# Kernel tuning notes

Hardware: AMD Instinct MI355X
Metric: run time of the kernel (lower is better)

The kernel has to match this reference:

```python
import jax, jax.numpy as jnp
import numpy as np

D_MODEL = 2048
NUM_HEADS = 16
D_K = D_MODEL // NUM_HEADS


def setup_inputs() -> dict:
    key = jax.random.key(0)
    ks = jax.random.split(key, 12)
    B, S, D = 2, 2048, D_MODEL
    s = 1.0 / np.sqrt(D)
    return {
        "q": jax.random.normal(ks[0], (B, S, D), jnp.float32),
        "k": jax.random.normal(ks[1], (B, S, D), jnp.float32),
        "v": jax.random.normal(ks[2], (B, S, D), jnp.float32),
        "Wq": jax.random.normal(ks[3], (D, D), jnp.float32) * s,
        "bq": jax.random.normal(ks[4], (D,), jnp.float32) * 0.01,
        "Wk": jax.random.normal(ks[5], (D, D), jnp.float32) * s,
        "bk": jax.random.normal(ks[6], (D,), jnp.float32) * 0.01,
        "Wv": jax.random.normal(ks[7], (D, D), jnp.float32) * s,
        "bv": jax.random.normal(ks[8], (D,), jnp.float32) * 0.01,
        "Wo": jax.random.normal(ks[9], (D, D), jnp.float32) * s,
        "bo": jax.random.normal(ks[10], (D,), jnp.float32) * 0.01,
    }


def reference(q, k, v, Wq, bq, Wk, bk, Wv, bv, Wo, bo):
    B, S, D = q.shape
    H, dk = NUM_HEADS, D_K

    def proj(x, W, b):
        # Linear then split heads -> [B, H, S, dk]
        y = jnp.einsum('bsd,df->bsf', x, W) + b
        return y.reshape(B, -1, H, dk).transpose(0, 2, 1, 3)

    Q = proj(q, Wq, bq)
    K = proj(k, Wk, bk)
    V = proj(v, Wv, bv)

    scores = jnp.einsum('bhqd,bhkd->bhqk', Q, K) / jnp.sqrt(jnp.float32(dk))
    attn = jax.nn.softmax(scores, axis=-1)  # dropout is identity (eval)
    out = jnp.einsum('bhqk,bhkd->bhqd', attn, V)
    out = out.transpose(0, 2, 1, 3).reshape(B, -1, D)
    return jnp.einsum('bsd,df->bsf', out, Wo) + bo
```

## Files before the change

### kernel.cpp

```cpp
#include <hip/hip_runtime.h>
#include <hip/hip_bf16.h>
#include <stdint.h>

typedef float  f32x4  __attribute__((ext_vector_type(4)));
typedef float  f32x16 __attribute__((ext_vector_type(16)));
typedef short  s16x8  __attribute__((ext_vector_type(8)));

#define D_MODEL 2048
#define NHEADS  16
#define DK      128
#define BATCH   2
#define SEQ     2048
#define MROWS   (BATCH*SEQ)

__device__ __forceinline__ unsigned short f2bf(float f) {
  union { float f; unsigned int u; } v; v.f = f;
  unsigned int r = v.u + 0x7FFFu + ((v.u >> 16) & 1u);
  return (unsigned short)(r >> 16);
}

__device__ __forceinline__ unsigned int packbf_c(float lo, float hi) {
  __hip_bfloat16 l = __float2bfloat16(lo);
  __hip_bfloat16 h = __float2bfloat16(hi);
  unsigned short lu, hu;
  __builtin_memcpy(&lu, &l, 2);
  __builtin_memcpy(&hu, &h, 2);
  return (unsigned int)lu | ((unsigned int)hu << 16);
}

__device__ __forceinline__ void async16(const void* g, void* l) {
  __builtin_amdgcn_global_load_lds(
      (const __attribute__((address_space(1))) unsigned int*)g,
      (__attribute__((address_space(3))) unsigned int*)l,
      16, 0, 0);
}

__global__ __launch_bounds__(256) void f2b3_kernel(const float* __restrict__ q,
                                                   const float* __restrict__ k,
                                                   const float* __restrict__ v,
                                                   unsigned short* __restrict__ qb,
                                                   unsigned short* __restrict__ kb,
                                                   unsigned short* __restrict__ vb) {
  const float* s; unsigned short* d;
  switch (blockIdx.y) {
    case 0:  s = q; d = qb; break;
    case 1:  s = k; d = kb; break;
    default: s = v; d = vb; break;
  }
  int i = blockIdx.x * 256 + threadIdx.x;
  const float4* s4 = (const float4*)s;
  float4 a = s4[2*i];
  float4 b = s4[2*i+1];
  s16x8 o;
  o[0] = (short)f2bf(a.x); o[1] = (short)f2bf(a.y);
  o[2] = (short)f2bf(a.z); o[3] = (short)f2bf(a.w);
  o[4] = (short)f2bf(b.x); o[5] = (short)f2bf(b.y);
  o[6] = (short)f2bf(b.z); o[7] = (short)f2bf(b.w);
  *(s16x8*)(d + 8*(size_t)i) = o;
}

__global__ __launch_bounds__(256) void wtrans_kernel(const float* __restrict__ Wq,
                                                     const float* __restrict__ Wk,
                                                     const float* __restrict__ Wv,
                                                     const float* __restrict__ Wo,
                                                     unsigned short* __restrict__ WqT,
                                                     unsigned short* __restrict__ WkT,
                                                     unsigned short* __restrict__ WvT,
                                                     unsigned short* __restrict__ WoT) {
  const float* W; unsigned short* Wt;
  switch (blockIdx.z) {
    case 0:  W = Wq; Wt = WqT; break;
    case 1:  W = Wk; Wt = WkT; break;
    case 2:  W = Wv; Wt = WvT; break;
    default: W = Wo; Wt = WoT; break;
  }
  __shared__ float tl[32][33];
  int x = threadIdx.x, y = threadIdx.y;
  int n0 = blockIdx.x * 32, k0 = blockIdx.y * 32;
  #pragma unroll
  for (int j = 0; j < 32; j += 8)
    tl[y + j][x] = W[(size_t)(k0 + y + j) * D_MODEL + n0 + x];
  __syncthreads();
  #pragma unroll
  for (int j = 0; j < 32; j += 8)
    Wt[(size_t)(n0 + y + j) * D_MODEL + k0 + x] = f2bf(tl[x][y + j]);
}

__device__ __forceinline__ void gemm3b_core(const unsigned short* __restrict__ A,
                                            const unsigned short* __restrict__ Bt,
                                            const float* __restrict__ bias,
                                            void* __restrict__ Cout,
                                            int N, int K, int mode, float scale,
                                            int m0, int n0, char* lds) {
  const int t  = threadIdx.x;
  const int l  = t & 63, w = t >> 6;
  const int wm = w >> 1, wn = w & 1;
  const int lr = l & 15, lg = l >> 4;

  auto STAGE = [&](int slot, int kt) {
    char* Ad = lds + slot*49152;
    char* Bd = lds + slot*49152 + 32768;
    #pragma unroll
    for (int i = 0; i < 4; ++i) {
      int c = t + 512*i;
      int row = c >> 3, crs = (c & 7) ^ (row & 7);
      async16(A + (size_t)(m0 + row)*K + kt*64 + crs*8, Ad + c*16);
    }
    #pragma unroll
    for (int i = 0; i < 2; ++i) {
      int c = t + 512*i;
      int row = c >> 3, crs = (c & 7) ^ (row & 7);
      async16(Bt + (size_t)(n0 + row)*K + kt*64 + crs*8, Bd + c*16);
    }
  };

  const int NT = K >> 6;
  STAGE(0, 0);
  STAGE(1, 1);
  asm volatile("s_waitcnt vmcnt(6)" ::: "memory");
  __builtin_amdgcn_s_barrier();

  f32x4 acc[4][4] = {};

  for (int kt = 0; kt < NT; ++kt) {
    if (kt + 2 < NT) STAGE((kt + 2) % 3, kt + 2);
    const char* Ac = lds + (kt % 3)*49152;
    const char* Bc = lds + (kt % 3)*49152 + 32768;

    #pragma unroll
    for (int ks = 0; ks < 2; ++ks) {
      const int cb = ks*64 + lg*16;
      s16x8 af[4], bf[4];
      #pragma unroll
      for (int mf = 0; mf < 4; ++mf) {
        int row = wm*64 + mf*16 + lr;
        af[mf] = *(const s16x8*)(Ac + row*128 + (cb ^ ((row & 7) << 4)));
      }
      #pragma unroll
      for (int nf = 0; nf < 4; ++nf) {
        int row = wn*64 + nf*16 + lr;
        bf[nf] = *(const s16x8*)(Bc + row*128 + (cb ^ ((row & 7) << 4)));
      }
      __builtin_amdgcn_s_setprio(1);
      #pragma unroll
      for (int mf = 0; mf < 4; ++mf)
        #pragma unroll
        for (int nf = 0; nf < 4; ++nf)
          acc[mf][nf] = __builtin_amdgcn_mfma_f32_16x16x32_bf16(af[mf], bf[nf], acc[mf][nf], 0, 0, 0);
      __builtin_amdgcn_s_setprio(0);
    }

    if (kt + 1 < NT) {
      if (kt + 2 < NT) asm volatile("s_waitcnt vmcnt(6)" ::: "memory");
      else             asm volatile("s_waitcnt vmcnt(0)" ::: "memory");
      __builtin_amdgcn_s_barrier();
    }
  }

  if (mode == 0) {
    float* C = (float*)Cout;
    #pragma unroll
    for (int nf = 0; nf < 4; ++nf) {
      int col = n0 + wn*64 + nf*16 + lr;
      float bv = bias[col];
      #pragma unroll
      for (int mf = 0; mf < 4; ++mf) {
        int rowb = m0 + wm*64 + mf*16 + lg*4;
        #pragma unroll
        for (int r = 0; r < 4; ++r)
          C[(size_t)(rowb + r)*N + col] = (acc[mf][nf][r] + bv) * scale;
      }
    }
  } else if (mode == 1) {
    unsigned short* C = (unsigned short*)Cout;
    #pragma unroll
    for (int nf = 0; nf < 4; ++nf) {
      int col = n0 + wn*64 + nf*16 + lr;
      float bv = bias[col];
      int h = col >> 7, dkk = col & 127;
      #pragma unroll
      for (int mf = 0; mf < 4; ++mf) {
        int rowb = m0 + wm*64 + mf*16 + lg*4;
        #pragma unroll
        for (int r = 0; r < 4; ++r) {
          int row = rowb + r;
          int b = row >> 11, s = row & 2047;
          C[((size_t)((b*NHEADS + h)*SEQ + s))*DK + dkk] = f2bf((acc[mf][nf][r] + bv) * scale);
        }
      }
    }
  } else {
    unsigned short* C = (unsigned short*)Cout;
    #pragma unroll
    for (int nf = 0; nf < 4; ++nf) {
      int col = n0 + wn*64 + nf*16 + lr;
      float bv = bias[col];
      int h = col >> 7, dkk = col & 127;
      #pragma unroll
      for (int mf = 0; mf < 4; ++mf) {
        int rowb = m0 + wm*64 + mf*16 + lg*4;
        #pragma unroll
        for (int r = 0; r < 4; ++r) {
          int row = rowb + r;
          int b = row >> 11, s = row & 2047;
          C[((size_t)((b*NHEADS + h)*DK + dkk))*SEQ + s] = f2bf((acc[mf][nf][r] + bv) * scale);
        }
      }
    }
  }
}

__device__ __forceinline__ void swz_mn(int& m0, int& n0) {
  int lin = blockIdx.y * 16 + blockIdx.x;
  int xcd = lin & 7;
  int pos = lin >> 3;
  n0 = (xcd*2 + (pos & 1)) * 128;
  m0 = (pos >> 1) * 256;
}

__global__ __launch_bounds__(512) void gemm256_qkv(const unsigned short* __restrict__ qb,
                                                   const unsigned short* __restrict__ kb,
                                                   const unsigned short* __restrict__ vb,
                                                   const unsigned short* __restrict__ WT,
                                                   const float* __restrict__ bq,
                                                   const float* __restrict__ bk,
                                                   const float* __restrict__ bv,
                                                   unsigned short* __restrict__ Hout,
                                                   float qscale) {
  __shared__ char lds[147456];
  const int z = blockIdx.z;
  const unsigned short* A = (z == 0) ? qb : (z == 1) ? kb : vb;
  const float* bias       = (z == 0) ? bq : (z == 1) ? bk : bv;
  const float scale       = (z == 0) ? qscale : 1.0f;
  const int   mode        = (z == 2) ? 2 : 1;
  const unsigned short* Bt = WT + (size_t)z * D_MODEL * D_MODEL;
  unsigned short* Cout     = Hout + (size_t)z * MROWS * D_MODEL;
  int m0, n0; swz_mn(m0, n0);
  gemm3b_core(A, Bt, bias, Cout, D_MODEL, D_MODEL, mode, scale, m0, n0, lds);
}

__global__ __launch_bounds__(512) void gemm256_out(const unsigned short* __restrict__ A,
                                                   const unsigned short* __restrict__ Bt,
                                                   const float* __restrict__ bias,
                                                   float* __restrict__ Cout) {
  __shared__ char lds[147456];
  int m0, n0; swz_mn(m0, n0);
  gemm3b_core(A, Bt, bias, Cout, D_MODEL, D_MODEL, 0, 1.0f, m0, n0, lds);
}

__global__ __launch_bounds__(256, 2) void attn_kernel(const unsigned short* __restrict__ Q,
                                                      const unsigned short* __restrict__ K,
                                                      const unsigned short* __restrict__ Vt_g,
                                                      unsigned short* __restrict__ O) {
  __shared__ char lds[64*256 + 2*16384];
  unsigned short* Kl = (unsigned short*)lds;

  const int t  = threadIdx.x;
  const int l  = t & 63, w = t >> 6;
  const int q_ = l & 31, hi = l >> 5;
  const int bh = blockIdx.y;
  const int b  = bh >> 4, h = bh & 15;
  const int q0 = blockIdx.x * 128;

  const unsigned short* Qp = Q    + (size_t)bh * SEQ * DK;
  const unsigned short* Kp = K    + (size_t)bh * SEQ * DK;
  const unsigned short* Vp = Vt_g + (size_t)bh * DK * SEQ;

  const int qrow = q0 + w*32 + q_;
  s16x8 aq[8];
  #pragma unroll
  for (int kk = 0; kk < 8; ++kk)
    aq[kk] = *(const s16x8*)(Qp + (size_t)qrow*DK + kk*16 + hi*8);

  f32x16 accO[4] = {};
  float m = -INFINITY, L = 0.f;

  const int NT = SEQ/64;

  auto stageK = [&](int kv0) {
    #pragma unroll
    for (int i = 0; i < 4; ++i) {
      int c   = t + 256*i;
      int row = c >> 4;
      int sb  = ((c & 15) << 4) ^ ((row & 15) << 4);
      async16((const char*)(Kp + (size_t)(kv0 + row)*DK) + sb, (char*)Kl + c*16);
    }
  };
  auto stageV = [&](int kv0, int buf) {
    char* Vd = lds + 16384 + buf*16384;
    #pragma unroll
    for (int i = 0; i < 4; ++i) {
      int c   = t + 256*i;
      int row = c >> 3;
      int sb  = ((c & 7) << 4) ^ ((row & 7) << 4);
      async16((const char*)(Vp + (size_t)row*SEQ + kv0) + sb, Vd + c*16);
    }
  };

  stageK(0);
  stageV(0, 0);
  asm volatile("" ::: "memory");

  for (int tt = 0; tt < NT; ++tt) {
    __syncthreads();

    f32x16 S0 = {}, S1 = {};
    __builtin_amdgcn_s_setprio(1);
    #pragma unroll
    for (int t2 = 0; t2 < 2; ++t2) {
      int krow = t2*32 + q_;
      const char* kb = (const char*)Kl + krow*256;
      int swz = (krow & 15) << 4;
      #pragma unroll
      for (int kk = 0; kk < 8; ++kk) {
        s16x8 kf = *(const s16x8*)(kb + ((kk*32 + hi*16) ^ swz));
        if (t2 == 0) S0 = __builtin_amdgcn_mfma_f32_32x32x16_bf16(kf, aq[kk], S0, 0, 0, 0);
        else         S1 = __builtin_amdgcn_mfma_f32_32x32x16_bf16(kf, aq[kk], S1, 0, 0, 0);
      }
    }
    __builtin_amdgcn_s_setprio(0);
    __syncthreads();

    if (tt + 1 < NT) {
      stageK((tt + 1) * 64);
      stageV((tt + 1) * 64, (tt + 1) & 1);
      asm volatile("" ::: "memory");
    }

    f32x16 mx;
    #pragma unroll
    for (int r = 0; r < 16; ++r) mx[r] = fmaxf(S0[r], S1[r]);
    float m8_[8];
    #pragma unroll
    for (int r = 0; r < 8; ++r) m8_[r] = fmaxf(mx[r], mx[r+8]);
    float m4a = fmaxf(m8_[0], m8_[4]), m4b = fmaxf(m8_[1], m8_[5]);
    float m4c = fmaxf(m8_[2], m8_[6]), m4d = fmaxf(m8_[3], m8_[7]);
    float pmax = fmaxf(fmaxf(m4a, m4b), fmaxf(m4c, m4d));
    pmax = fmaxf(pmax, __shfl_xor(pmax, 32, 64));

    if (!__all(pmax <= m + 11.0f)) {
      float mnew = fmaxf(m, pmax);
      float corr = exp2f(m - mnew);
      m = mnew;
      L *= corr;
      #pragma unroll
      for (int sub = 0; sub < 4; ++sub)
        #pragma unroll
        for (int r = 0; r < 16; ++r) accO[sub][r] *= corr;
    }

    float rs0 = 0.f, rs1 = 0.f, rs2 = 0.f, rs3 = 0.f;
    #pragma unroll
    for (int r = 0; r < 4; ++r) {
      float a0 = exp2f(S0[r]    - m); S0[r]    = a0; rs0 += a0;
      float a1 = exp2f(S0[r+4]  - m); S0[r+4]  = a1; rs1 += a1;
      float a2 = exp2f(S0[r+8]  - m); S0[r+8]  = a2; rs2 += a2;
      float a3 = exp2f(S0[r+12] - m); S0[r+12] = a3; rs3 += a3;
      float b0 = exp2f(S1[r]    - m); S1[r]    = b0; rs0 += b0;
      float b1 = exp2f(S1[r+4]  - m); S1[r+4]  = b1; rs1 += b1;
      float b2 = exp2f(S1[r+8]  - m); S1[r+8]  = b2; rs2 += b2;
      float b3 = exp2f(S1[r+12] - m); S1[r+12] = b3; rs3 += b3;
    }
    float rs = (rs0 + rs1) + (rs2 + rs3);
    rs += __shfl_xor(rs, 32, 64);
    L += rs;

    s16x8 PB[4];
    #pragma unroll
    for (int t2 = 0; t2 < 2; ++t2) {
      #pragma unroll
      for (int half = 0; half < 2; ++half) {
        int bse = half*8;
        unsigned int pkA01, pkA23, pkB01, pkB23;
        if (t2 == 0) {
          pkA01 = packbf_c(S0[bse+0], S0[bse+1]);
          pkA23 = packbf_c(S0[bse+2], S0[bse+3]);
          pkB01 = packbf_c(S0[bse+4], S0[bse+5]);
          pkB23 = packbf_c(S0[bse+6], S0[bse+7]);
        } else {
          pkA01 = packbf_c(S1[bse+0], S1[bse+1]);
          pkA23 = packbf_c(S1[bse+2], S1[bse+3]);
          pkB01 = packbf_c(S1[bse+4], S1[bse+5]);
          pkB23 = packbf_c(S1[bse+6], S1[bse+7]);
        }
        unsigned int xA01 = __shfl_xor(pkA01, 32, 64);
        unsigned int xA23 = __shfl_xor(pkA23, 32, 64);
        unsigned int xB01 = __shfl_xor(pkB01, 32, 64);
        unsigned int xB23 = __shfl_xor(pkB23, 32, 64);
        union { unsigned int u[4]; s16x8 v; } f;
        f.u[0] = hi ? xB01 : pkA01;
        f.u[1] = hi ? xB23 : pkA23;
        f.u[2] = hi ? pkB01 : xA01;
        f.u[3] = hi ? pkB23 : xA23;
        PB[t2*2 + half] = f.v;
      }
    }

    const char* Vc = lds + 16384 + (tt & 1)*16384;
    __builtin_amdgcn_s_setprio(1);
    #pragma unroll
    for (int sub = 0; sub < 4; ++sub) {
      int row = sub*32 + q_;
      const char* vb2 = Vc + row*128;
      int swz = (row & 7) << 4;
      #pragma unroll
      for (int kk = 0; kk < 4; ++kk) {
        s16x8 vf = *(const s16x8*)(vb2 + ((kk*32 + hi*16) ^ swz));
        accO[sub] = __builtin_amdgcn_mfma_f32_32x32x16_bf16(vf, PB[kk], accO[sub], 0, 0, 0);
      }
    }
    __builtin_amdgcn_s_setprio(0);
  }

  __syncthreads();
  unsigned short* Ob = (unsigned short*)lds + (size_t)w*4096;
  float inv = 1.0f / L;
  #pragma unroll
  for (int sub = 0; sub < 4; ++sub)
    #pragma unroll
    for (int j = 0; j < 8; ++j) {
      unsigned int pw = packbf_c(accO[sub][2*j]*inv, accO[sub][2*j+1]*inv);
      int dv = sub*32 + (j&1)*2 + ((j>>1)*8) + 4*hi;
      *(unsigned int*)((char*)Ob + q_*256 + ((dv*2) ^ ((q_ & 15) << 4))) = pw;
    }
  asm volatile("s_waitcnt lgkmcnt(0)" ::: "memory");
  size_t gbase = ((size_t)(b*SEQ + q0 + w*32 + q_))*D_MODEL + h*DK;
  #pragma unroll
  for (int p = 0; p < 8; ++p) {
    int chunk = hi + 2*p;
    s16x8 ov = *(const s16x8*)((char*)Ob + q_*256 + ((chunk*16) ^ ((q_ & 15) << 4)));
    *(s16x8*)(O + gbase + chunk*8) = ov;
  }
}

extern "C" void kernel_launch(void* const* d_in, const int* in_sizes, int n_in,
                              void* d_out, int out_size, void* d_ws, size_t ws_size,
                              hipStream_t stream) {
  const float* q  = (const float*)d_in[0];
  const float* k  = (const float*)d_in[1];
  const float* v  = (const float*)d_in[2];
  const float* Wq = (const float*)d_in[3];
  const float* bq = (const float*)d_in[4];
  const float* Wk = (const float*)d_in[5];
  const float* bk = (const float*)d_in[6];
  const float* Wv = (const float*)d_in[7];
  const float* bv = (const float*)d_in[8];
  const float* Wo = (const float*)d_in[9];
  const float* bo = (const float*)d_in[10];
  float* out = (float*)d_out;

  char* ws = (char*)d_ws;
  const size_t SZT = (size_t)MROWS * D_MODEL * 2;
  const size_t SZW = (size_t)D_MODEL * D_MODEL * 2;

  unsigned short* qb  = (unsigned short*)(ws);
  unsigned short* kb  = (unsigned short*)(ws + SZT);
  unsigned short* vb  = (unsigned short*)(ws + 2*SZT);
  unsigned short* WqT = (unsigned short*)(ws + 3*SZT);
  unsigned short* WkT = (unsigned short*)(ws + 3*SZT + SZW);
  unsigned short* WvT = (unsigned short*)(ws + 3*SZT + 2*SZW);
  unsigned short* WoT = (unsigned short*)(ws + 3*SZT + 3*SZW);
  unsigned short* Qh  = (unsigned short*)(ws + 3*SZT + 4*SZW);
  unsigned short* Kh  = (unsigned short*)(ws + 4*SZT + 4*SZW);
  unsigned short* Vh  = (unsigned short*)(ws + 5*SZT + 4*SZW);
  unsigned short* Oc  = qb;

  const int n8 = MROWS * D_MODEL / 8;
  f2b3_kernel<<<dim3(n8/256, 3), 256, 0, stream>>>(q, k, v, qb, kb, vb);
  wtrans_kernel<<<dim3(64, 64, 4), dim3(32, 8), 0, stream>>>(Wq, Wk, Wv, Wo, WqT, WkT, WvT, WoT);

  const float qscale = 0.1275174308f;
  gemm256_qkv<<<dim3(16, 16, 3), 512, 0, stream>>>(qb, kb, vb, WqT, bq, bk, bv, Qh, qscale);

  attn_kernel<<<dim3(SEQ/128, BATCH*NHEADS), 256, 0, stream>>>(Qh, Kh, Vh, Oc);

  gemm256_out<<<dim3(16, 16), 512, 0, stream>>>(Oc, WoT, bo, out);
}
```

Baseline: 306.2 us.

## Merge prep kernels and double-buffer K/V tiles in attention

Folds the fp32-to-bf16 conversion of activations and the weight transpose into a single launch, removing one kernel launch and the gap between the two. The attention kernel now double-buffers both K and V tiles and prefetches two tiles ahead, waiting with partial vmcnt instead of a full sync. This lets global loads overlap with the QK^T and PV MFMA work at the cost of more LDS per block (64KB), which may reduce occupancy.

```diff
diff --git a/kernel.cpp b/kernel.cpp
--- a/kernel.cpp
+++ b/kernel.cpp
@@ -35,55 +35,51 @@
       16, 0, 0);
 }
 
-__global__ __launch_bounds__(256) void f2b3_kernel(const float* __restrict__ q,
+__global__ __launch_bounds__(256) void prep_kernel(const float* __restrict__ q,
                                                    const float* __restrict__ k,
                                                    const float* __restrict__ v,
+                                                   const float* __restrict__ Wq,
+                                                   const float* __restrict__ Wk,
+                                                   const float* __restrict__ Wv,
+                                                   const float* __restrict__ Wo,
                                                    unsigned short* __restrict__ qb,
                                                    unsigned short* __restrict__ kb,
-                                                   unsigned short* __restrict__ vb) {
-  const float* s; unsigned short* d;
-  switch (blockIdx.y) {
-    case 0:  s = q; d = qb; break;
-    case 1:  s = k; d = kb; break;
-    default: s = v; d = vb; break;
+                                                   unsigned short* __restrict__ vb,
+                                                   unsigned short* __restrict__ WT) {
+  const int t = threadIdx.x;
+  if (blockIdx.x < 12288) {
+    int bz = blockIdx.x / 4096;
+    int bx = blockIdx.x - bz * 4096;
+    const float* s = (bz == 0) ? q : (bz == 1) ? k : v;
+    unsigned short* d = (bz == 0) ? qb : (bz == 1) ? kb : vb;
+    int i = bx * 256 + t;
+    const float4* s4 = (const float4*)s;
+    float4 a = s4[2*i];
+    float4 b = s4[2*i+1];
+    s16x8 o;
+    o[0] = (short)f2bf(a.x); o[1] = (short)f2bf(a.y);
+    o[2] = (short)f2bf(a.z); o[3] = (short)f2bf(a.w);
+    o[4] = (short)f2bf(b.x); o[5] = (short)f2bf(b.y);
+    o[6] = (short)f2bf(b.z); o[7] = (short)f2bf(b.w);
+    *(s16x8*)(d + 8*(size_t)i) = o;
+  } else {
+    int lin = blockIdx.x - 12288;
+    int z   = lin >> 12;
+    int rem = lin & 4095;
+    int bx  = rem & 63, by = rem >> 6;
+    const float* W = (z == 0) ? Wq : (z == 1) ? Wk : (z == 2) ? Wv : Wo;
+    unsigned short* Wt = WT + (size_t)z * D_MODEL * D_MODEL;
+    __shared__ float tl[32][33];
+    int x = t & 31, y = t >> 5;
+    int n0 = bx * 32, k0 = by * 32;
+    #pragma unroll
+    for (int j = 0; j < 32; j += 8)
+      tl[y + j][x] = W[(size_t)(k0 + y + j) * D_MODEL + n0 + x];
+    __syncthreads();
+    #pragma unroll
+    for (int j = 0; j < 32; j += 8)
+      Wt[(size_t)(n0 + y + j) * D_MODEL + k0 + x] = f2bf(tl[x][y + j]);
   }
-  int i = blockIdx.x * 256 + threadIdx.x;
-  const float4* s4 = (const float4*)s;
-  float4 a = s4[2*i];
-  float4 b = s4[2*i+1];
-  s16x8 o;
-  o[0] = (short)f2bf(a.x); o[1] = (short)f2bf(a.y);
-  o[2] = (short)f2bf(a.z); o[3] = (short)f2bf(a.w);
-  o[4] = (short)f2bf(b.x); o[5] = (short)f2bf(b.y);
-  o[6] = (short)f2bf(b.z); o[7] = (short)f2bf(b.w);
-  *(s16x8*)(d + 8*(size_t)i) = o;
-}
-
-__global__ __launch_bounds__(256) void wtrans_kernel(const float* __restrict__ Wq,
-                                                     const float* __restrict__ Wk,
-                                                     const float* __restrict__ Wv,
-                                                     const float* __restrict__ Wo,
-                                                     unsigned short* __restrict__ WqT,
-                                                     unsigned short* __restrict__ WkT,
-                                                     unsigned short* __restrict__ WvT,
-                                                     unsigned short* __restrict__ WoT) {
-  const float* W; unsigned short* Wt;
-  switch (blockIdx.z) {
-    case 0:  W = Wq; Wt = WqT; break;
-    case 1:  W = Wk; Wt = WkT; break;
-    case 2:  W = Wv; Wt = WvT; break;
-    default: W = Wo; Wt = WoT; break;
-  }
-  __shared__ float tl[32][33];
-  int x = threadIdx.x, y = threadIdx.y;
-  int n0 = blockIdx.x * 32, k0 = blockIdx.y * 32;
-  #pragma unroll
-  for (int j = 0; j < 32; j += 8)
-    tl[y + j][x] = W[(size_t)(k0 + y + j) * D_MODEL + n0 + x];
-  __syncthreads();
-  #pragma unroll
-  for (int j = 0; j < 32; j += 8)
-    Wt[(size_t)(n0 + y + j) * D_MODEL + k0 + x] = f2bf(tl[x][y + j]);
 }
 
 __device__ __forceinline__ void gemm3b_core(const unsigned short* __restrict__ A,
@@ -252,8 +248,7 @@
                                                       const unsigned short* __restrict__ K,
                                                       const unsigned short* __restrict__ Vt_g,
                                                       unsigned short* __restrict__ O) {
-  __shared__ char lds[64*256 + 2*16384];
-  unsigned short* Kl = (unsigned short*)lds;
+  __shared__ char lds[4*16384];
 
   const int t  = threadIdx.x;
   const int l  = t & 63, w = t >> 6;
@@ -277,17 +272,18 @@
 
   const int NT = SEQ/64;
 
-  auto stageK = [&](int kv0) {
+  auto stageK = [&](int kv0, int buf) {
+    char* Kd = lds + buf*16384;
     #pragma unroll
     for (int i = 0; i < 4; ++i) {
       int c   = t + 256*i;
       int row = c >> 4;
       int sb  = ((c & 15) << 4) ^ ((row & 15) << 4);
-      async16((const char*)(Kp + (size_t)(kv0 + row)*DK) + sb, (char*)Kl + c*16);
+      async16((const char*)(Kp + (size_t)(kv0 + row)*DK) + sb, Kd + c*16);
     }
   };
   auto stageV = [&](int kv0, int buf) {
-    char* Vd = lds + 16384 + buf*16384;
+    char* Vd = lds + 32768 + buf*16384;
     #pragma unroll
     for (int i = 0; i < 4; ++i) {
       int c   = t + 256*i;
@@ -297,19 +293,24 @@
     }
   };
 
-  stageK(0);
-  stageV(0, 0);
+  stageK(0, 0);  stageV(0, 0);
+  stageK(64, 1); stageV(64, 1);
   asm volatile("" ::: "memory");
 
   for (int tt = 0; tt < NT; ++tt) {
-    __syncthreads();
+    if (tt + 1 < NT) asm volatile("s_waitcnt vmcnt(8)" ::: "memory");
+    else             asm volatile("s_waitcnt vmcnt(0)" ::: "memory");
+    __builtin_amdgcn_s_barrier();
+
+    const char* Kl = lds + (tt & 1)*16384;
+    const char* Vc = lds + 32768 + (tt & 1)*16384;
 
     f32x16 S0 = {}, S1 = {};
     __builtin_amdgcn_s_setprio(1);
     #pragma unroll
     for (int t2 = 0; t2 < 2; ++t2) {
       int krow = t2*32 + q_;
-      const char* kb = (const char*)Kl + krow*256;
+      const char* kb = Kl + krow*256;
       int swz = (krow & 15) << 4;
       #pragma unroll
       for (int kk = 0; kk < 8; ++kk) {
@@ -319,13 +320,6 @@
       }
     }
     __builtin_amdgcn_s_setprio(0);
-    __syncthreads();
-
-    if (tt + 1 < NT) {
-      stageK((tt + 1) * 64);
-      stageV((tt + 1) * 64, (tt + 1) & 1);
-      asm volatile("" ::: "memory");
-    }
 
     f32x16 mx;
     #pragma unroll
@@ -396,7 +390,6 @@
       }
     }
 
-    const char* Vc = lds + 16384 + (tt & 1)*16384;
     __builtin_amdgcn_s_setprio(1);
     #pragma unroll
     for (int sub = 0; sub < 4; ++sub) {
@@ -410,6 +403,13 @@
       }
     }
     __builtin_amdgcn_s_setprio(0);
+
+    if (tt + 2 < NT) {
+      __builtin_amdgcn_s_barrier();
+      stageK((tt + 2) * 64, tt & 1);
+      stageV((tt + 2) * 64, tt & 1);
+      asm volatile("" ::: "memory");
+    }
   }
 
   __syncthreads();
@@ -457,17 +457,13 @@
   unsigned short* kb  = (unsigned short*)(ws + SZT);
   unsigned short* vb  = (unsigned short*)(ws + 2*SZT);
   unsigned short* WqT = (unsigned short*)(ws + 3*SZT);
-  unsigned short* WkT = (unsigned short*)(ws + 3*SZT + SZW);
-  unsigned short* WvT = (unsigned short*)(ws + 3*SZT + 2*SZW);
   unsigned short* WoT = (unsigned short*)(ws + 3*SZT + 3*SZW);
   unsigned short* Qh  = (unsigned short*)(ws + 3*SZT + 4*SZW);
   unsigned short* Kh  = (unsigned short*)(ws + 4*SZT + 4*SZW);
   unsigned short* Vh  = (unsigned short*)(ws + 5*SZT + 4*SZW);
   unsigned short* Oc  = qb;
 
-  const int n8 = MROWS * D_MODEL / 8;
-  f2b3_kernel<<<dim3(n8/256, 3), 256, 0, stream>>>(q, k, v, qb, kb, vb);
-  wtrans_kernel<<<dim3(64, 64, 4), dim3(32, 8), 0, stream>>>(Wq, Wk, Wv, Wo, WqT, WkT, WvT, WoT);
+  prep_kernel<<<dim3(12288 + 16384), 256, 0, stream>>>(q, k, v, Wq, Wk, Wv, Wo, qb, kb, vb, WqT);
 
   const float qscale = 0.1275174308f;
   gemm256_qkv<<<dim3(16, 16, 3), 512, 0, stream>>>(qb, kb, vb, WqT, bq, bk, bv, Qh, qscale);
```

Result: no change. 308.7 us (+0.8%).
